# Kernel tuning notes

Hardware: AMD Instinct MI355X
Metric: run time of the kernel (lower is better)

## Reference

```python
import jax, jax.numpy as jnp
import numpy as np

H = 7500.0
N, T, C = 64, 65536, 4


def setup_inputs() -> dict:
    key = jax.random.key(0)
    k1, k2, k3 = jax.random.split(key, 3)
    # predictions roughly in [0, h]
    output_rsd = jax.random.uniform(k1, (N, T, C), dtype=jnp.float32) * H
    # targets span [-0.25h, 1.25h] so >h, <0, in-range, and early bins are all hit
    u = jax.random.uniform(k2, (N, T, C), dtype=jnp.float32)
    target_rsd = (u * 1.5 - 0.25) * H
    z = jax.random.uniform(k3, (N, T, C), dtype=jnp.float32)
    target_rsd = jnp.where(z < 0.05, 0.0, target_rsd)
    return {"output_rsd": output_rsd, "target_rsd": target_rsd}


def _nanmean2(a, b):
    # nanmean over a stacked pair, elementwise
    va = ~jnp.isnan(a)
    vb = ~jnp.isnan(b)
    s = jnp.where(va, a, 0.0) + jnp.where(vb, b, 0.0)
    c = va.astype(a.dtype) + vb.astype(a.dtype)
    return jnp.where(c > 0, s / jnp.maximum(c, 1.0), jnp.nan)


def reference(output_rsd, target_rsd):
    h = jnp.float32(H)
    if target_rsd.ndim < 3:
        target_rsd = target_rsd[..., None]
    # clamp out-of-range targets to h (same as torch.where((t>h)|(t<0), h, t))
    t = jnp.where((target_rsd > h) | (target_rsd < 0), h, target_rsd)
    d = jnp.abs(output_rsd - t)  # [N, T, C]

    def masked_mean(mask):
        m = mask.astype(d.dtype)
        c = m.sum(axis=1)                  # [N, C]
        s = (d * m).sum(axis=1)            # [N, C]
        return jnp.where(c > 0, s / jnp.maximum(c, 1.0), jnp.nan)

    m_o = masked_mean(t == h)                          # over-horizon
    m_in = masked_mean((t < h) & (t > 0))              # in-horizon
    m_u = masked_mean(t == 0)                          # target exactly 0
    m_e = masked_mean((t < 0.1 * h) & (t > 0))         # early (<0.1h)

    in_comb = _nanmean2(m_u, m_in)   # per-(n,c) inMAE
    w = _nanmean2(m_o, in_comb)      # per-(n,c) wMAE

    wMAE = jnp.nanmean(w)
    inMAE = jnp.nanmean(in_comb)
    oMAE = jnp.nanmean(m_o)
    eMAE = jnp.nanmean(m_e)
    return (wMAE, inMAE, oMAE, eMAE)
```

## Files before the change

### kernel.cpp

```cpp
#include <hip/hip_runtime.h>
#include <math.h>

#define H_VAL   7500.0f
#define EH_VAL  750.0f
#define N_DIM   64
#define T_DIM   65536
#define BLOCKS_PER_N 32
#define NBLOCKS (N_DIM * BLOCKS_PER_N)
#define THREADS 256
#define T_PER_BLOCK (T_DIM / BLOCKS_PER_N)
#define ITERS (T_PER_BLOCK / THREADS)

__device__ __forceinline__ float dev_nan() { return __uint_as_float(0x7fc00000u); }
__device__ __forceinline__ bool is_nan(float x) { return x != x; }


template <bool ATOMIC>
__global__ __launch_bounds__(THREADS) void mae_stage1(
        const float* __restrict__ outp, const float* __restrict__ tgtp,
        float* __restrict__ ws) {
    const int n = blockIdx.x / BLOCKS_PER_N;
    const int slice = blockIdx.x % BLOCKS_PER_N;
    const int t0 = slice * T_PER_BLOCK;
    const int tid = threadIdx.x;
    const float h = H_VAL;
    const float eh = EH_VAL;

    float w[16];
    #pragma unroll
    for (int i = 0; i < 16; ++i) w[i] = 0.0f;
    unsigned cnt[4] = {0u, 0u, 0u, 0u};

    const float4* o4 = reinterpret_cast<const float4*>(outp) + (size_t)n * T_DIM;
    const float4* t4 = reinterpret_cast<const float4*>(tgtp) + (size_t)n * T_DIM;

    auto proc = [&](const float4& ov, const float4& tv) {
        const float os[4] = {ov.x, ov.y, ov.z, ov.w};
        const float ts[4] = {tv.x, tv.y, tv.z, tv.w};
        #pragma unroll
        for (int c = 0; c < 4; ++c) {
            const float traw = ts[c];
            const bool bo = (traw >= h) || (traw < 0.0f);
            const float tc = bo ? h : traw;
            const float d = fabsf(os[c] - tc);
            const bool bu = (traw == 0.0f);
            const bool be = (traw > 0.0f) && (traw < eh);
            w[c * 4 + 0] += d;
            w[c * 4 + 1] += bo ? d : 0.0f;
            w[c * 4 + 2] += bu ? d : 0.0f;
            w[c * 4 + 3] += be ? d : 0.0f;
            cnt[c] += (bo ? 1u : 0u) + (bu ? (1u << 10) : 0u) + (be ? (1u << 20) : 0u);
        }
    };

#define IDX(i) ((size_t)(t0 + (i) * THREADS + tid))
    float4 a0o = o4[IDX(0)], a1o = o4[IDX(1)];
    float4 a0t = t4[IDX(0)], a1t = t4[IDX(1)];
    #pragma unroll
    for (int it = 0; it < ITERS; it += 2) {
        float4 b0o = a0o, b1o = a1o, b0t = a0t, b1t = a1t;
        if (it + 2 < ITERS) {
            b0o = o4[IDX(it + 2)]; b1o = o4[IDX(it + 3)];
            b0t = t4[IDX(it + 2)]; b1t = t4[IDX(it + 3)];
        }
        proc(a0o, a0t);
        proc(a1o, a1t);
        a0o = b0o; a1o = b1o; a0t = b0t; a1t = b1t;
    }
#undef IDX

    const int lane = tid & 63;
    #pragma unroll
    for (int r = 0; r < 4; ++r) {
        const int dist = 1 << r;
        const bool hi = (lane >> r) & 1;
        const int c16 = 8 >> r;
        #pragma unroll
        for (int j = 0; j < c16; ++j) {
            const float send = hi ? w[j] : w[j + c16];
            const float recv = __shfl_xor(send, dist, 64);
            w[j] = (hi ? w[j + c16] : w[j]) + recv;
        }
    }
    w[0] += __shfl_xor(w[0], 16, 64);
    w[0] += __shfl_xor(w[0], 32, 64);
    const int l4 = lane & 15;
    const int slot = ((l4 & 1) << 3) | (((l4 >> 1) & 1) << 2) |
                     (((l4 >> 2) & 1) << 1) | ((l4 >> 3) & 1);

    #pragma unroll
    for (int r = 0; r < 2; ++r) {
        const int dist = 1 << r;
        const bool hi = (lane >> r) & 1;
        const int c4 = 2 >> r;
        #pragma unroll
        for (int j = 0; j < c4; ++j) {
            const unsigned send = hi ? cnt[j] : cnt[j + c4];
            const unsigned recv = __shfl_xor(send, dist, 64);
            cnt[j] = (hi ? cnt[j + c4] : cnt[j]) + recv;
        }
    }
    cnt[0] += __shfl_xor(cnt[0], 4, 64);
    cnt[0] += __shfl_xor(cnt[0], 8, 64);
    cnt[0] += __shfl_xor(cnt[0], 16, 64);
    cnt[0] += __shfl_xor(cnt[0], 32, 64);
    const int slot2 = ((lane & 1) << 1) | ((lane >> 1) & 1);

    __shared__ float    lsum[4][16];
    __shared__ unsigned lcnt[4][4];
    const int wave = tid >> 6;
    if (lane < 16) lsum[wave][slot] = w[0];
    if (lane < 4)  lcnt[wave][slot2] = cnt[0];
    __syncthreads();

    if (tid < 16) {
        const float s = lsum[0][tid] + lsum[1][tid] + lsum[2][tid] + lsum[3][tid];
        if (ATOMIC) {
            const int c = tid >> 2, k = tid & 3;
            atomicAdd(&ws[n * 32 + c * 8 + k], s);
        } else {
            ws[blockIdx.x * 28 + tid] = s;
        }
    } else if (tid < 28) {
        const int j = tid - 16, f = j >> 2, c = j & 3;
        const unsigned v = ((lcnt[0][c] >> (10 * f)) & 1023u) +
                           ((lcnt[1][c] >> (10 * f)) & 1023u) +
                           ((lcnt[2][c] >> (10 * f)) & 1023u) +
                           ((lcnt[3][c] >> (10 * f)) & 1023u);
        const float fv = (float)v;
        if (ATOMIC) {
            atomicAdd(&ws[n * 32 + c * 8 + 4 + f], fv);
        } else {
            ws[blockIdx.x * 28 + tid] = fv;
        }
    }
}

template <bool ATOMIC>
__global__ __launch_bounds__(256) void mae_stage2(
        const float* __restrict__ ws, float* __restrict__ outp) {
    const int i = threadIdx.x;
    const int n = i >> 2, c = i & 3;

    float a[7];
    if (ATOMIC) {
        const float* p = &ws[n * 32 + c * 8];
        #pragma unroll
        for (int k = 0; k < 4; ++k) a[k] = p[k];
        #pragma unroll
        for (int f = 0; f < 3; ++f) a[4 + f] = p[4 + f];
    } else {
        #pragma unroll
        for (int k = 0; k < 7; ++k) a[k] = 0.0f;
        for (int s = 0; s < BLOCKS_PER_N; ++s) {
            const float* p = &ws[(size_t)(n * BLOCKS_PER_N + s) * 28];
            #pragma unroll
            for (int k = 0; k < 4; ++k) a[k] += p[c * 4 + k];
            #pragma unroll
            for (int f = 0; f < 3; ++f) a[4 + f] += p[16 + f * 4 + c];
        }
    }

    const float sum_all = a[0], sum_o = a[1], sum_u = a[2], sum_e = a[3];
    const float cnt_o = a[4], cnt_u = a[5], cnt_e = a[6];
    const float cnt_in = (float)T_DIM - cnt_o - cnt_u;
    const float sum_in = sum_all - sum_o - sum_u;

    const float m_o  = (cnt_o  > 0.0f) ? sum_o  / cnt_o  : dev_nan();
    const float m_in = (cnt_in > 0.0f) ? sum_in / cnt_in : dev_nan();
    const float m_u  = (cnt_u  > 0.0f) ? sum_u  / cnt_u  : dev_nan();
    const float m_e  = (cnt_e  > 0.0f) ? sum_e  / cnt_e  : dev_nan();

    auto nm2 = [](float x, float y) {
        const bool vx = !is_nan(x), vy = !is_nan(y);
        const float s  = (vx ? x : 0.0f) + (vy ? y : 0.0f);
        const float cc = (vx ? 1.0f : 0.0f) + (vy ? 1.0f : 0.0f);
        return (cc > 0.0f) ? s / cc : dev_nan();
    };
    const float in_comb = nm2(m_u, m_in);
    const float wv      = nm2(m_o, in_comb);

    float vals[4] = {wv, in_comb, m_o, m_e};
    float sums[4], cnts[4];
    #pragma unroll
    for (int j = 0; j < 4; ++j) {
        const bool valid = !is_nan(vals[j]);
        sums[j] = valid ? vals[j] : 0.0f;
        cnts[j] = valid ? 1.0f : 0.0f;
    }
    #pragma unroll
    for (int j = 0; j < 4; ++j) {
        #pragma unroll
        for (int off = 32; off > 0; off >>= 1) {
            sums[j] += __shfl_down(sums[j], off, 64);
            cnts[j] += __shfl_down(cnts[j], off, 64);
        }
    }
    __shared__ float ls[4][8];
    const int wave = threadIdx.x >> 6;
    const int lane = threadIdx.x & 63;
    if (lane == 0) {
        #pragma unroll
        for (int j = 0; j < 4; ++j) { ls[wave][j] = sums[j]; ls[wave][j + 4] = cnts[j]; }
    }
    __syncthreads();
    if (threadIdx.x == 0) {
        #pragma unroll
        for (int j = 0; j < 4; ++j) {
            const float s  = ls[0][j] + ls[1][j] + ls[2][j] + ls[3][j];
            const float cc = ls[0][j + 4] + ls[1][j + 4] + ls[2][j + 4] + ls[3][j + 4];
            outp[j] = (cc > 0.0f) ? s / cc : dev_nan();
        }
    }
}

extern "C" void kernel_launch(void* const* d_in, const int* in_sizes, int n_in,
                              void* d_out, int out_size, void* d_ws, size_t ws_size,
                              hipStream_t stream) {
    const float* out_rsd = (const float*)d_in[0];
    const float* tgt_rsd = (const float*)d_in[1];
    float* outv = (float*)d_out;
    float* ws = (float*)d_ws;

    const size_t partials_bytes = (size_t)NBLOCKS * 28 * sizeof(float);
    if (ws_size >= partials_bytes) {
        mae_stage1<false><<<NBLOCKS, THREADS, 0, stream>>>(out_rsd, tgt_rsd, ws);
        mae_stage2<false><<<1, 256, 0, stream>>>(ws, outv);
    } else {
        hipMemsetAsync(ws, 0, N_DIM * 32 * sizeof(float), stream);
        mae_stage1<true><<<NBLOCKS, THREADS, 0, stream>>>(out_rsd, tgt_rsd, ws);
        mae_stage2<true><<<1, 256, 0, stream>>>(ws, outv);
    }
}
```

Baseline: 32.15 us.

## Stream inputs through LDS with async global_load_lds triple buffering

Replaces the register double-buffered float4 loads with direct global-to-LDS async copies into a three-stage shared buffer, using explicit vmcnt waits to keep two tiles in flight while computing the current one. The aim is deeper memory-level parallelism and lower register pressure for this bandwidth-bound reduction. It adds 24KB of LDS per block, which may reduce occupancy, and relies on per-wave LDS ordering without a barrier, which is correct only because each wave reads back the region it staged itself.

```diff
diff --git a/kernel.cpp b/kernel.cpp
--- a/kernel.cpp
+++ b/kernel.cpp
@@ -9,10 +9,20 @@
 #define NBLOCKS (N_DIM * BLOCKS_PER_N)
 #define THREADS 256
 #define T_PER_BLOCK (T_DIM / BLOCKS_PER_N)
-#define ITERS (T_PER_BLOCK / THREADS)
+#define NTILES 8
+#define TILE_T 256
 
 __device__ __forceinline__ float dev_nan() { return __uint_as_float(0x7fc00000u); }
 __device__ __forceinline__ bool is_nan(float x) { return x != x; }
+
+typedef __attribute__((address_space(3))) unsigned       lds_uint;
+typedef __attribute__((address_space(1))) const unsigned g_uint;
+
+__device__ __forceinline__ void stage16(const float4* g, float4* l) {
+    __builtin_amdgcn_global_load_lds((g_uint*)g, (lds_uint*)l, 16, 0, 0);
+}
+
+#define WAITVM(N) asm volatile("s_waitcnt vmcnt(" #N ")" ::: "memory")
 
 
 template <bool ATOMIC>
@@ -23,6 +33,7 @@
     const int slice = blockIdx.x % BLOCKS_PER_N;
     const int t0 = slice * T_PER_BLOCK;
     const int tid = threadIdx.x;
+    const int lane = tid & 63;
     const float h = H_VAL;
     const float eh = EH_VAL;
 
@@ -33,6 +44,9 @@
 
     const float4* o4 = reinterpret_cast<const float4*>(outp) + (size_t)n * T_DIM;
     const float4* t4 = reinterpret_cast<const float4*>(tgtp) + (size_t)n * T_DIM;
+
+    __shared__ float4 buf[3][2][THREADS];
+    const int wbase = tid & ~63;
 
     auto proc = [&](const float4& ov, const float4& tv) {
         const float os[4] = {ov.x, ov.y, ov.z, ov.w};
@@ -53,23 +67,29 @@
         }
     };
 
-#define IDX(i) ((size_t)(t0 + (i) * THREADS + tid))
-    float4 a0o = o4[IDX(0)], a1o = o4[IDX(1)];
-    float4 a0t = t4[IDX(0)], a1t = t4[IDX(1)];
-    #pragma unroll
-    for (int it = 0; it < ITERS; it += 2) {
-        float4 b0o = a0o, b1o = a1o, b0t = a0t, b1t = a1t;
-        if (it + 2 < ITERS) {
-            b0o = o4[IDX(it + 2)]; b1o = o4[IDX(it + 3)];
-            b0t = t4[IDX(it + 2)]; b1t = t4[IDX(it + 3)];
-        }
-        proc(a0o, a0t);
-        proc(a1o, a1t);
-        a0o = b0o; a1o = b1o; a0t = b0t; a1t = b1t;
-    }
-#undef IDX
-
-    const int lane = tid & 63;
+#define STAGE(T)  do { \
+        const int gi = t0 + (T) * TILE_T + tid; \
+        stage16(o4 + gi, &buf[(T) % 3][0][wbase]); \
+        stage16(t4 + gi, &buf[(T) % 3][1][wbase]); \
+    } while (0)
+#define PROC(T)   do { \
+        const float4 ov = buf[(T) % 3][0][tid]; \
+        const float4 tv = buf[(T) % 3][1][tid]; \
+        proc(ov, tv); \
+    } while (0)
+
+    STAGE(0); STAGE(1);
+    STAGE(2); WAITVM(4); PROC(0);
+    STAGE(3); WAITVM(4); PROC(1);
+    STAGE(4); WAITVM(4); PROC(2);
+    STAGE(5); WAITVM(4); PROC(3);
+    STAGE(6); WAITVM(4); PROC(4);
+    STAGE(7); WAITVM(4); PROC(5);
+    WAITVM(2); PROC(6);
+    WAITVM(0); PROC(7);
+#undef STAGE
+#undef PROC
+
     #pragma unroll
     for (int r = 0; r < 4; ++r) {
         const int dist = 1 << r;
```

Result: slower. 33.01 us (+2.7%).

## Batch loads in bursts of four and count masks with wave ballots

Applied to the files above, without the earlier changes.

Replaces the two-deep software-prefetch loop with bursts that issue four float4 loads per input before computing, raising memory-level parallelism per thread. Per-lane packed counters and their shuffle reduction are replaced by wave-wide ballot+popcount counts kept as scalar values, so only lane 0 writes counts to shared memory. Ballots add scalar work per element and the burst structure drops cross-iteration overlap between loads and compute.

```diff
diff --git a/kernel.cpp b/kernel.cpp
--- a/kernel.cpp
+++ b/kernel.cpp
@@ -10,6 +10,7 @@
 #define THREADS 256
 #define T_PER_BLOCK (T_DIM / BLOCKS_PER_N)
 #define ITERS (T_PER_BLOCK / THREADS)
+#define BURST 4
 
 __device__ __forceinline__ float dev_nan() { return __uint_as_float(0x7fc00000u); }
 __device__ __forceinline__ bool is_nan(float x) { return x != x; }
@@ -23,53 +24,53 @@
     const int slice = blockIdx.x % BLOCKS_PER_N;
     const int t0 = slice * T_PER_BLOCK;
     const int tid = threadIdx.x;
+    const int lane = tid & 63;
     const float h = H_VAL;
     const float eh = EH_VAL;
 
     float w[16];
     #pragma unroll
     for (int i = 0; i < 16; ++i) w[i] = 0.0f;
-    unsigned cnt[4] = {0u, 0u, 0u, 0u};
+    unsigned co[4] = {0u, 0u, 0u, 0u};
+    unsigned cu_[4] = {0u, 0u, 0u, 0u};
+    unsigned ce[4] = {0u, 0u, 0u, 0u};
 
     const float4* o4 = reinterpret_cast<const float4*>(outp) + (size_t)n * T_DIM;
     const float4* t4 = reinterpret_cast<const float4*>(tgtp) + (size_t)n * T_DIM;
 
-    auto proc = [&](const float4& ov, const float4& tv) {
-        const float os[4] = {ov.x, ov.y, ov.z, ov.w};
-        const float ts[4] = {tv.x, tv.y, tv.z, tv.w};
-        #pragma unroll
-        for (int c = 0; c < 4; ++c) {
-            const float traw = ts[c];
-            const bool bo = (traw >= h) || (traw < 0.0f);
-            const float tc = bo ? h : traw;
-            const float d = fabsf(os[c] - tc);
-            const bool bu = (traw == 0.0f);
-            const bool be = (traw > 0.0f) && (traw < eh);
-            w[c * 4 + 0] += d;
-            w[c * 4 + 1] += bo ? d : 0.0f;
-            w[c * 4 + 2] += bu ? d : 0.0f;
-            w[c * 4 + 3] += be ? d : 0.0f;
-            cnt[c] += (bo ? 1u : 0u) + (bu ? (1u << 10) : 0u) + (be ? (1u << 20) : 0u);
-        }
-    };
-
-#define IDX(i) ((size_t)(t0 + (i) * THREADS + tid))
-    float4 a0o = o4[IDX(0)], a1o = o4[IDX(1)];
-    float4 a0t = t4[IDX(0)], a1t = t4[IDX(1)];
-    #pragma unroll
-    for (int it = 0; it < ITERS; it += 2) {
-        float4 b0o = a0o, b1o = a1o, b0t = a0t, b1t = a1t;
-        if (it + 2 < ITERS) {
-            b0o = o4[IDX(it + 2)]; b1o = o4[IDX(it + 3)];
-            b0t = t4[IDX(it + 2)]; b1t = t4[IDX(it + 3)];
-        }
-        proc(a0o, a0t);
-        proc(a1o, a1t);
-        a0o = b0o; a1o = b1o; a0t = b0t; a1t = b1t;
-    }
-#undef IDX
-
-    const int lane = tid & 63;
+    #pragma unroll
+    for (int half = 0; half < ITERS / BURST; ++half) {
+        float4 lo[BURST], lt[BURST];
+        #pragma unroll
+        for (int j = 0; j < BURST; ++j)
+            lo[j] = o4[t0 + (half * BURST + j) * THREADS + tid];
+        #pragma unroll
+        for (int j = 0; j < BURST; ++j)
+            lt[j] = t4[t0 + (half * BURST + j) * THREADS + tid];
+
+        #pragma unroll
+        for (int j = 0; j < BURST; ++j) {
+            const float os[4] = {lo[j].x, lo[j].y, lo[j].z, lo[j].w};
+            const float ts[4] = {lt[j].x, lt[j].y, lt[j].z, lt[j].w};
+            #pragma unroll
+            for (int c = 0; c < 4; ++c) {
+                const float traw = ts[c];
+                const bool bo = (traw >= h) || (traw < 0.0f);
+                const float tc = bo ? h : traw;
+                const float d = fabsf(os[c] - tc);
+                const bool bu = (traw == 0.0f);
+                const bool be = (traw > 0.0f) && (traw < eh);
+                w[c * 4 + 0] += d;
+                w[c * 4 + 1] += bo ? d : 0.0f;
+                w[c * 4 + 2] += bu ? d : 0.0f;
+                w[c * 4 + 3] += be ? d : 0.0f;
+                co[c]  += (unsigned)__popcll(__ballot(bo));
+                cu_[c] += (unsigned)__popcll(__ballot(bu));
+                ce[c]  += (unsigned)__popcll(__ballot(be));
+            }
+        }
+    }
+
     #pragma unroll
     for (int r = 0; r < 4; ++r) {
         const int dist = 1 << r;
@@ -88,29 +89,18 @@
     const int slot = ((l4 & 1) << 3) | (((l4 >> 1) & 1) << 2) |
                      (((l4 >> 2) & 1) << 1) | ((l4 >> 3) & 1);
 
-    #pragma unroll
-    for (int r = 0; r < 2; ++r) {
-        const int dist = 1 << r;
-        const bool hi = (lane >> r) & 1;
-        const int c4 = 2 >> r;
-        #pragma unroll
-        for (int j = 0; j < c4; ++j) {
-            const unsigned send = hi ? cnt[j] : cnt[j + c4];
-            const unsigned recv = __shfl_xor(send, dist, 64);
-            cnt[j] = (hi ? cnt[j + c4] : cnt[j]) + recv;
-        }
-    }
-    cnt[0] += __shfl_xor(cnt[0], 4, 64);
-    cnt[0] += __shfl_xor(cnt[0], 8, 64);
-    cnt[0] += __shfl_xor(cnt[0], 16, 64);
-    cnt[0] += __shfl_xor(cnt[0], 32, 64);
-    const int slot2 = ((lane & 1) << 1) | ((lane >> 1) & 1);
-
     __shared__ float    lsum[4][16];
-    __shared__ unsigned lcnt[4][4];
+    __shared__ unsigned lcnt[4][12];
     const int wave = tid >> 6;
     if (lane < 16) lsum[wave][slot] = w[0];
-    if (lane < 4)  lcnt[wave][slot2] = cnt[0];
+    if (lane == 0) {
+        #pragma unroll
+        for (int c = 0; c < 4; ++c) {
+            lcnt[wave][0 * 4 + c] = co[c];
+            lcnt[wave][1 * 4 + c] = cu_[c];
+            lcnt[wave][2 * 4 + c] = ce[c];
+        }
+    }
     __syncthreads();
 
     if (tid < 16) {
@@ -123,10 +113,7 @@
         }
     } else if (tid < 28) {
         const int j = tid - 16, f = j >> 2, c = j & 3;
-        const unsigned v = ((lcnt[0][c] >> (10 * f)) & 1023u) +
-                           ((lcnt[1][c] >> (10 * f)) & 1023u) +
-                           ((lcnt[2][c] >> (10 * f)) & 1023u) +
-                           ((lcnt[3][c] >> (10 * f)) & 1023u);
+        const unsigned v = lcnt[0][j] + lcnt[1][j] + lcnt[2][j] + lcnt[3][j];
         const float fv = (float)v;
         if (ATOMIC) {
             atomicAdd(&ws[n * 32 + c * 8 + 4 + f], fv);
```

Result: slower. 41.05 us (+27.7%).
